# Performance work log

Hardware: AMD Instinct MI355X
Metric: run time of the kernel (lower is better)

## Reference

```python
import jax, jax.numpy as jnp
import numpy as np

HEAD_DIM = 128
N_HEADS = 32
ROPE_DIM = 64
TOPK = 1024
B, S, HID, QLORA = 1, 2048, 4096, 1536
LN_EPS = 1e-5  # torch nn.LayerNorm default


def _hadamard_matrix(n):
    H = np.array([[1.0]], dtype=np.float32)
    while H.shape[0] < n:
        H = np.block([[H, H], [H, -H]])
    return jnp.asarray(H)

_H128 = _hadamard_matrix(HEAD_DIM)
_FWHT_SCALE = HEAD_DIM ** -0.5


def rotate_activation(x):
    # Fast Walsh-Hadamard transform == x @ H_sylvester, scaled by dim**-0.5
    return (x @ _H128) * _FWHT_SCALE


def rope_non_interleaved(x, cos, sin):
    # x: [..., rope_dim]; cos/sin: broadcastable [..., rope_dim/2]
    half = x.shape[-1] // 2
    x1, x2 = x[..., :half], x[..., half:]
    return jnp.concatenate([x1 * cos - x2 * sin, x1 * sin + x2 * cos], axis=-1)


def setup_inputs() -> dict:
    key = jax.random.key(0)
    ks = jax.random.split(key, 8)
    hidden_states = jax.random.normal(ks[0], (B, S, HID), jnp.float32)
    q_compressed = jax.random.normal(ks[1], (B, S, QLORA), jnp.float32)
    # rotary cos/sin for rope_dim=64 (standard concat layout)
    pos = jnp.arange(S, dtype=jnp.float32)
    inv_freq = 1.0 / (10000.0 ** (jnp.arange(0, ROPE_DIM, 2, dtype=jnp.float32) / ROPE_DIM))
    ang = pos[:, None] * inv_freq[None, :]  # [S, 32]
    cos = jnp.tile(jnp.cos(ang), (1, 2))[None]  # [1, S, 64]
    sin = jnp.tile(jnp.sin(ang), (1, 2))[None]
    # additive causal mask [B, S, S]
    causal = jnp.tril(jnp.ones((S, S), jnp.bool_))
    attention_mask = jnp.where(causal, 0.0, -1e9).astype(jnp.float32)[None]
    Wq_b = jax.random.normal(ks[2], (QLORA, N_HEADS * HEAD_DIM), jnp.float32) * (QLORA ** -0.5)
    Wk = jax.random.normal(ks[3], (HID, HEAD_DIM), jnp.float32) * (HID ** -0.5)
    k_gamma = jnp.ones((HEAD_DIM,), jnp.float32)
    k_beta = jnp.zeros((HEAD_DIM,), jnp.float32)
    Ww = jax.random.normal(ks[4], (HID, N_HEADS), jnp.float32) * (HID ** -0.5)
    return {"hidden_states": hidden_states, "q_compressed": q_compressed, "cos": cos,
            "sin": sin, "attention_mask": attention_mask, "Wq_b": Wq_b, "Wk": Wk,
            "k_gamma": k_gamma, "k_beta": k_beta, "Ww": Ww}


def reference(hidden_states, q_compressed, cos, sin, attention_mask, Wq_b, Wk, k_gamma, k_beta, Ww):
    b, s, _ = hidden_states.shape
    softmax_scale = HEAD_DIM ** -0.5
    # queries: [b, s, H, D]
    q = (q_compressed @ Wq_b).reshape(b, s, N_HEADS, HEAD_DIM)
    q_rope, q_nope = q[..., :ROPE_DIM], q[..., ROPE_DIM:]
    # keys: single shared head, LayerNorm(k)
    k = hidden_states @ Wk  # [b, s, D]
    mu = jnp.mean(k, axis=-1, keepdims=True)
    var = jnp.mean(jnp.square(k - mu), axis=-1, keepdims=True)
    k = (k - mu) * jax.lax.rsqrt(var + LN_EPS) * k_gamma + k_beta
    k_rope, k_nope = k[..., :ROPE_DIM], k[..., ROPE_DIM:]
    # non-interleaved RoPE (cos/sin truncated to half_dim=32)
    half = ROPE_DIM // 2
    c, sn = cos[..., :half], sin[..., :half]
    q_rope = rope_non_interleaved(q_rope, c[:, :, None, :], sn[:, :, None, :])
    k_rope = rope_non_interleaved(k_rope, c, sn)
    q = jnp.concatenate([q_rope, q_nope], axis=-1)
    k = jnp.concatenate([k_rope, k_nope], axis=-1)
    # Hadamard activation rotation
    q = rotate_activation(q)
    k = rotate_activation(k)
    # I_{t,s} = sum_h w_{t,h} * ReLU(q_{t,h} . k_s) * scale
    scores = jax.nn.relu(jnp.einsum('bthd,bsd->bths', q, k)) * softmax_scale
    weights = hidden_states @ Ww  # [b, t, H]
    index_scores = jnp.einsum('bths,bth->bts', scores, weights)
    index_scores = index_scores + attention_mask
    topk = min(TOPK, s)
    _, topk_indices = jax.lax.top_k(index_scores, topk)  # [b, s, topk]
    return topk_indices, index_scores
```

## Files before the change

### kernel.cpp

```cpp
#include <hip/hip_runtime.h>
#include <stdint.h>

#define S_LEN 2048
#define HID 4096
#define QLORA 1536
#define NH 32
#define HD 128
#define TOPK_N 1024
#define NEG_INF -1000000000.0f
#define INV_SQRT_HD 0.08838834764831844f

typedef __attribute__((ext_vector_type(8))) short short8;
typedef __attribute__((ext_vector_type(4))) short short4_;
typedef __attribute__((ext_vector_type(4))) float float4_;
typedef __attribute__((ext_vector_type(4))) unsigned uint4_;
typedef __attribute__((ext_vector_type(4))) int int4_;
typedef __attribute__((ext_vector_type(2))) int int2_;

__device__ __forceinline__ short f2bf(float x) {
  union { float f; unsigned u; } v; v.f = x;
  unsigned r = v.u + 0x7FFFu + ((v.u >> 16) & 1u);
  return (short)(r >> 16);
}

__device__ __forceinline__ unsigned f2ord(float x) {
  union { float f; unsigned u; } v; v.f = x;
  return v.u ^ (0x80000000u | (unsigned)((int)v.u >> 31));
}

__device__ __forceinline__ void gload_lds16(const void* g, void* l) {
  __builtin_amdgcn_global_load_lds((const __attribute__((address_space(1))) unsigned int*)g,
                                   (__attribute__((address_space(3))) unsigned int*)l, 16, 0, 0);
}

__global__ __launch_bounds__(256) void prep_kernel(
    const float* __restrict__ hidden, short* __restrict__ hidb,
    const float* __restrict__ qc, char* __restrict__ qc8,
    float* __restrict__ kacc,
    const float* __restrict__ wqb, char* __restrict__ wq8T,
    const float* __restrict__ wk, const float* __restrict__ ww,
    short* __restrict__ kwT) {
  __shared__ __align__(8) char stile[4352];
  int bid = blockIdx.x;
  const int tid = threadIdx.x;
  if (bid < 8192) {
    int i = bid * 256 + tid;
    float4 v = ((const float4*)hidden)[i];
    short4_ o;
    o[0] = f2bf(v.x); o[1] = f2bf(v.y); o[2] = f2bf(v.z); o[3] = f2bf(v.w);
    ((short4_*)hidb)[i] = o;
    return;
  }
  if (bid < 9728) {
    int i = (bid - 8192) * 256 + tid;
    float4 f0 = ((const float4*)qc)[i * 2];
    float4 f1 = ((const float4*)qc)[i * 2 + 1];
    int lo = 0, hi = 0;
    lo = __builtin_amdgcn_cvt_pk_fp8_f32(f0.x, f0.y, lo, 0);
    lo = __builtin_amdgcn_cvt_pk_fp8_f32(f0.z, f0.w, lo, 1);
    hi = __builtin_amdgcn_cvt_pk_fp8_f32(f1.x, f1.y, hi, 0);
    hi = __builtin_amdgcn_cvt_pk_fp8_f32(f1.z, f1.w, hi, 1);
    ((int2_*)qc8)[i] = (int2_){lo, hi};
    return;
  }
  if (bid < 10048) {
    int i = (bid - 9728) * 256 + tid;
    ((float4_*)kacc)[i] = (float4_){0.f, 0.f, 0.f, 0.f};
    return;
  }
  if (bid < 13120) {
    char (*t8)[33] = (char(*)[33])stile;
    int b = bid - 10048;
    int k0 = (b >> 7) * 64, n0 = (b & 127) * 32;
    #pragma unroll
    for (int i = 0; i < 8; i++) {
      int e = tid + i * 256;
      int r = e >> 5, c = e & 31;
      float x = wqb[(size_t)(k0 + r) * HID + n0 + c];
      t8[r][c] = (char)__builtin_amdgcn_cvt_pk_fp8_f32(x, x, 0, 0);
    }
    __syncthreads();
    int nl = tid >> 3, jk = (tid & 7) * 8;
    union { char c[8]; long l; } o;
    #pragma unroll
    for (int j = 0; j < 8; j++) o.c[j] = t8[jk + j][nl];
    *(long*)(wq8T + (size_t)(n0 + nl) * QLORA + k0 + jk) = o.l;
    return;
  }
  short (*tile)[33] = (short(*)[33])stile;
  const float* in; short* out; int R, C, bx, by;
  if (bid < 13632) {
    int b2 = bid - 13120;
    in = wk; out = kwT; R = HID; C = HD; bx = b2 & 3; by = b2 >> 2;
  } else {
    int b3 = bid - 13632;
    in = ww; out = kwT + 128 * HID; R = HID; C = NH; bx = 0; by = b3;
  }
  int c0 = bx * 32, r0 = by * 32;
  int tx = tid & 31, ty = tid >> 5;
  #pragma unroll
  for (int i = 0; i < 32; i += 8)
    tile[ty + i][tx] = f2bf(in[(size_t)(r0 + ty + i) * C + c0 + tx]);
  __syncthreads();
  #pragma unroll
  for (int i = 0; i < 32; i += 8)
    out[(size_t)(c0 + ty + i) * R + r0 + tx] = tile[tx][ty + i];
}

#define QSTAGE8(kt, Ad, Bd) do { \
  _Pragma("unroll") \
  for (int i = 0; i < 4; i++) { \
    int m = w * 32 + i * 8 + lr; \
    int gb = (kt) * 128 + ((lc ^ (m & 7)) << 4); \
    gload_lds16(qc8 + (size_t)(t0 + m) * QLORA + gb, (Ad) + (w * 32 + i * 8) * 128); \
    gload_lds16(wq8T + (size_t)(n0 + m) * QLORA + gb, (Bd) + (w * 32 + i * 8) * 128); \
  } \
} while (0)

#define QCOMPUTE8(Aq, Bq) do { \
  _Pragma("unroll") \
  for (int p = 0; p < 4; p++) { \
    int ch = p * 2 + (quad >> 1); \
    int lo8 = (quad & 1) * 8; \
    long a[2], b[8]; \
    _Pragma("unroll") \
    for (int mt = 0; mt < 2; mt++) { \
      int m = w * 32 + mt * 16 + l15; \
      a[mt] = *(const long*)((Aq) + m * 128 + ((ch ^ (m & 7)) << 4) + lo8); \
    } \
    _Pragma("unroll") \
    for (int nt = 0; nt < 8; nt++) { \
      int n = nt * 16 + l15; \
      b[nt] = *(const long*)((Bq) + n * 128 + ((ch ^ (n & 7)) << 4) + lo8); \
    } \
    _Pragma("unroll") \
    for (int mt = 0; mt < 2; mt++) \
      _Pragma("unroll") \
      for (int nt = 0; nt < 8; nt++) \
        acc[mt][nt] = __builtin_amdgcn_mfma_f32_16x16x32_fp8_fp8(a[mt], b[nt], acc[mt][nt], 0, 0, 0); \
  } \
} while (0)

__global__ __launch_bounds__(256, 2) void gemms_kernel(
    const char* __restrict__ qc8, const char* __restrict__ wq8T,
    const float* __restrict__ cosp, const float* __restrict__ sinp,
    short* __restrict__ qrot,
    const short* __restrict__ hidb, const short* __restrict__ kwT,
    float* __restrict__ kacc) {
  __shared__ __align__(16) char smem[65536];
  const int tid = threadIdx.x;
  const int w = tid >> 6, lane = tid & 63;
  const int l15 = lane & 15, quad = lane >> 4;
  const int lr = lane >> 3, lc = lane & 7;

  if (blockIdx.x < 512) {
    char* A0 = smem;
    char* B0 = smem + 16384;
    char* A1 = smem + 32768;
    char* B1 = smem + 49152;
    const int n0 = (blockIdx.x & 31) * 128;
    const int t0 = (blockIdx.x >> 5) * 128;

    float4_ acc[2][8];
    #pragma unroll
    for (int mt = 0; mt < 2; mt++)
      #pragma unroll
      for (int i = 0; i < 8; i++) acc[mt][i] = (float4_){0.f, 0.f, 0.f, 0.f};

    QSTAGE8(0, A0, B0);
    __syncthreads();
    for (int kt = 0; kt < 12; kt += 2) {
      QSTAGE8(kt + 1, A1, B1);
      QCOMPUTE8(A0, B0);
      __syncthreads();
      if (kt + 2 < 12) QSTAGE8(kt + 2, A0, B0);
      QCOMPUTE8(A1, B1);
      __syncthreads();
    }

    #pragma unroll
    for (int mt = 0; mt < 2; mt++) {
      #pragma unroll
      for (int r = 0; r < 4; r++) {
        const int trow = t0 + w * 32 + mt * 16 + quad * 4 + r;
        float v[8];
        #pragma unroll
        for (int nt = 0; nt < 8; nt++) v[nt] = acc[mt][nt][r];
        float cc0 = cosp[trow * 64 + l15], cc1 = cosp[trow * 64 + 16 + l15];
        float ss0 = sinp[trow * 64 + l15], ss1 = sinp[trow * 64 + 16 + l15];
        float r0 = v[0] * cc0 - v[2] * ss0, r1 = v[1] * cc1 - v[3] * ss1;
        float r2 = v[0] * ss0 + v[2] * cc0, r3 = v[1] * ss1 + v[3] * cc1;
        v[0] = r0; v[1] = r1; v[2] = r2; v[3] = r3;
        short* orow = qrot + (size_t)trow * HID + n0;
        #pragma unroll
        for (int nt = 0; nt < 8; nt++)
          orow[nt * 16 + l15] = f2bf(v[nt]);
      }
    }
  } else {
    short* Al = (short*)smem;
    short* Bl = (short*)(smem + 8192);
    const int b2 = blockIdx.x - 512;
    const int kc0 = (b2 & 7) * 512;
    const int m0g = (b2 >> 3) * 64;

    float4_ acc[10];
    #pragma unroll
    for (int i = 0; i < 10; i++) acc[i] = (float4_){0.f, 0.f, 0.f, 0.f};

    for (int k0 = kc0; k0 < kc0 + 512; k0 += 64) {
      #pragma unroll
      for (int i = 0; i < 2; i++) {
        int m = w * 16 + i * 8 + lr;
        int gk = k0 + ((lc ^ (m & 7)) << 3);
        gload_lds16(hidb + (size_t)(m0g + m) * HID + gk, Al + (w * 16 + i * 8) * 64);
      }
      #pragma unroll
      for (int i = 0; i < 5; i++) {
        int n = w * 40 + i * 8 + lr;
        int gk = k0 + ((lc ^ (n & 7)) << 3);
        gload_lds16(kwT + (size_t)n * HID + gk, Bl + (w * 40 + i * 8) * 64);
      }
      __syncthreads();
      #pragma unroll
      for (int kk = 0; kk < 64; kk += 32) {
        int ca = (kk >> 3) + quad;
        int ma = w * 16 + l15;
        short8 a = *(const short8*)(Al + ma * 64 + ((ca ^ (ma & 7)) << 3));
        #pragma unroll
        for (int nt = 0; nt < 10; nt++) {
          int n = nt * 16 + l15;
          short8 b = *(const short8*)(Bl + n * 64 + ((ca ^ (n & 7)) << 3));
          acc[nt] = __builtin_amdgcn_mfma_f32_16x16x32_bf16(a, b, acc[nt], 0, 0, 0);
        }
      }
      __syncthreads();
    }
    #pragma unroll
    for (int nt = 0; nt < 10; nt++)
      #pragma unroll
      for (int r = 0; r < 4; r++) {
        int row = m0g + w * 16 + quad * 4 + r;
        atomicAdd(&kacc[(size_t)row * 160 + nt * 16 + l15], acc[nt][r]);
      }
  }
}

__global__ __launch_bounds__(256) void ln_rope_kernel(
    const float* __restrict__ kacc, const float* __restrict__ gamma,
    const float* __restrict__ beta, const float* __restrict__ cosp,
    const float* __restrict__ sinp, short* __restrict__ krot) {
  const int tid = threadIdx.x;
  const int row = blockIdx.x * 16 + (tid >> 4);
  const int l16 = tid & 15;
  const int c0 = l16 * 8;
  const float* rp = kacc + (size_t)row * 160 + c0;
  float4 f0 = ((const float4*)rp)[0], f1 = ((const float4*)rp)[1];
  float v[8] = {f0.x, f0.y, f0.z, f0.w, f1.x, f1.y, f1.z, f1.w};
  float s = 0.f, ss = 0.f;
  #pragma unroll
  for (int j = 0; j < 8; j++) { s += v[j]; ss += v[j] * v[j]; }
  #pragma unroll
  for (int d = 1; d <= 8; d <<= 1) {
    s += __shfl_xor(s, d, 64); ss += __shfl_xor(ss, d, 64);
  }
  float mu = s * (1.0f / 128.0f);
  float var = ss * (1.0f / 128.0f) - mu * mu;
  float rs = rsqrtf(var + 1e-5f);
  #pragma unroll
  for (int j = 0; j < 8; j++)
    v[j] = (v[j] - mu) * rs * gamma[c0 + j] + beta[c0 + j];
  #pragma unroll
  for (int j = 0; j < 8; j++) {
    float p = __shfl_xor(v[j], 4, 64);
    if (l16 < 8) {
      int idx = (c0 + j) & 31;
      float c = cosp[row * 64 + idx], sn = sinp[row * 64 + idx];
      v[j] = v[j] * c + p * ((l16 < 4) ? -sn : sn);
    }
  }
  short8 o;
  #pragma unroll
  for (int j = 0; j < 8; j++) o[j] = f2bf(v[j]);
  *(short8*)(krot + (size_t)row * 128 + c0) = o;
}

__global__ __launch_bounds__(256, 2) void scores_kernel(
    const short* __restrict__ qrot, const short* __restrict__ krot,
    const float* __restrict__ kacc, float* __restrict__ isc) {
  __shared__ __align__(16) char smem[65536];
  short* buf0 = (short*)smem;
  short* buf1 = (short*)(smem + 32768);

  const int tid = threadIdx.x;
  const int w = tid >> 6, lane = tid & 63;
  const int l15 = lane & 15, quad = lane >> 4;
  const int wm = w >> 1, wn = w & 1;
  const int lr16 = lane >> 4, lc16 = lane & 15;

  const int bid = blockIdx.x;
  const int strip = (bid & 1) ? (511 - (bid >> 1)) : (bid >> 1);
  const int t0 = strip * 4;
  const int nsb = (t0 + 3) / 128 + 1;

  const short* Abase = qrot + (size_t)t0 * 32 * 128;
  #pragma unroll
  for (int i = 0; i < 8; i++) {
    int m = (w * 8 + i) * 4 + lr16;
    int gofs = m * 128 + ((lc16 ^ (m & 7)) << 3);
    gload_lds16(Abase + gofs, buf0 + (w * 8 + i) * 512);
    gload_lds16(krot + gofs, buf1 + (w * 8 + i) * 512);
  }
  __syncthreads();

  short8 af[4][4];
  #pragma unroll
  for (int k4 = 0; k4 < 4; k4++) {
    int ca = k4 * 4 + quad;
    #pragma unroll
    for (int mt = 0; mt < 4; mt++) {
      int m = wm * 64 + mt * 16 + l15;
      af[k4][mt] = *(const short8*)(buf0 + m * 128 + ((ca ^ (m & 7)) << 3));
    }
  }

  const int t_a = t0 + wm * 2, t_b = t_a + 1;
  float wq[4][4];
  #pragma unroll
  for (int mt = 0; mt < 4; mt++) {
    int tt = (mt < 2) ? t_a : t_b;
    #pragma unroll
    for (int r = 0; r < 4; r++)
      wq[mt][r] = kacc[(size_t)tt * 160 + 128 + (mt & 1) * 16 + quad * 4 + r];
  }
  __syncthreads();

  for (int sb = 0; sb < nsb; sb++) {
    short* cur = (sb & 1) ? buf0 : buf1;
    if (sb + 1 < nsb) {
      short* nxt = (sb & 1) ? buf1 : buf0;
      const short* Bbase = krot + (size_t)(sb + 1) * 128 * 128;
      #pragma unroll
      for (int i = 0; i < 8; i++) {
        int m = (w * 8 + i) * 4 + lr16;
        int gofs = m * 128 + ((lc16 ^ (m & 7)) << 3);
        gload_lds16(Bbase + gofs, nxt + (w * 8 + i) * 512);
      }
    }

    float4_ acc[4][4];
    #pragma unroll
    for (int mt = 0; mt < 4; mt++)
      #pragma unroll
      for (int nt = 0; nt < 4; nt++) acc[mt][nt] = (float4_){0.f, 0.f, 0.f, 0.f};

    #pragma unroll
    for (int k4 = 0; k4 < 4; k4++) {
      int ca = k4 * 4 + quad;
      short8 b[4];
      #pragma unroll
      for (int nt = 0; nt < 4; nt++) {
        int n = wn * 64 + nt * 16 + l15;
        b[nt] = *(const short8*)(cur + n * 128 + ((ca ^ (n & 7)) << 3));
      }
      #pragma unroll
      for (int mt = 0; mt < 4; mt++)
        #pragma unroll
        for (int nt = 0; nt < 4; nt++)
          acc[mt][nt] = __builtin_amdgcn_mfma_f32_16x16x32_bf16(af[k4][mt], b[nt], acc[mt][nt], 0, 0, 0);
    }

    #pragma unroll
    for (int nt = 0; nt < 4; nt++) {
      float pa = 0.f, pb = 0.f;
      #pragma unroll
      for (int r = 0; r < 4; r++) {
        pa += fmaxf(acc[0][nt][r], 0.f) * wq[0][r] + fmaxf(acc[1][nt][r], 0.f) * wq[1][r];
        pb += fmaxf(acc[2][nt][r], 0.f) * wq[2][r] + fmaxf(acc[3][nt][r], 0.f) * wq[3][r];
      }
      pa += __shfl_xor(pa, 16, 64); pa += __shfl_xor(pa, 32, 64);
      pb += __shfl_xor(pb, 16, 64); pb += __shfl_xor(pb, 32, 64);
      int s = sb * 128 + wn * 64 + nt * 16 + l15;
      if (quad == 0)
        isc[(size_t)t_a * S_LEN + s] = (s <= t_a) ? pa * INV_SQRT_HD : NEG_INF;
      else if (quad == 1)
        isc[(size_t)t_b * S_LEN + s] = (s <= t_b) ? pb * INV_SQRT_HD : NEG_INF;
    }

    __syncthreads();
  }

  if (wn == 0) {
    const int myrow = (lane < 32) ? t_a : t_b;
    const int l32 = lane & 31;
    float4_ nf = (float4_){NEG_INF, NEG_INF, NEG_INF, NEG_INF};
    float4_* rowp = (float4_*)(isc + (size_t)myrow * S_LEN);
    for (int i = nsb * 32 + l32; i < 512; i += 32) rowp[i] = nf;
  }
}

#define CEK(x, y, d) { if ((d) ? (v[x] < v[y]) : (v[x] > v[y])) { unsigned _t = v[x]; v[x] = v[y]; v[y] = _t; } }

__device__ __forceinline__ void shfl_phase(unsigned v[8], int j, int base, bool d) {
  const int delta = j >> 3;
  const bool keep_max = (((base & j) == 0) == d);
  #pragma unroll
  for (int r = 0; r < 8; r++) {
    unsigned pv = (unsigned)__shfl_xor((int)v[r], delta, 64);
    unsigned mx = v[r] > pv ? v[r] : pv;
    unsigned mn = v[r] > pv ? pv : v[r];
    v[r] = keep_max ? mx : mn;
  }
}

__device__ __forceinline__ void reg_phase(unsigned v[8], bool d) {
  CEK(0, 4, d); CEK(1, 5, d); CEK(2, 6, d); CEK(3, 7, d);
  CEK(0, 2, d); CEK(1, 3, d); CEK(4, 6, d); CEK(5, 7, d);
  CEK(0, 1, d); CEK(2, 3, d); CEK(4, 5, d); CEK(6, 7, d);
}

__device__ __forceinline__ int chswz(int c) { return c ^ ((c >> 3) & 7); }

__device__ __forceinline__ void lds_phase(unsigned v[8], unsigned* keys, int tid, int base,
                                          int j, bool d) {
  const int c0 = tid * 2, c1 = c0 + 1;
  ((uint4_*)keys)[chswz(c0)] = (uint4_){v[0], v[1], v[2], v[3]};
  ((uint4_*)keys)[chswz(c1)] = (uint4_){v[4], v[5], v[6], v[7]};
  __syncthreads();
  const int ptid = tid ^ (j >> 3);
  uint4_ u0 = ((uint4_*)keys)[chswz(ptid * 2)];
  uint4_ u1 = ((uint4_*)keys)[chswz(ptid * 2 + 1)];
  unsigned p[8] = {u0[0], u0[1], u0[2], u0[3], u1[0], u1[1], u1[2], u1[3]};
  const bool keep_max = (((base & j) == 0) == d);
  #pragma unroll
  for (int r = 0; r < 8; r++) {
    unsigned mx = v[r] > p[r] ? v[r] : p[r];
    unsigned mn = v[r] > p[r] ? p[r] : v[r];
    v[r] = keep_max ? mx : mn;
  }
  __syncthreads();
}

__global__ __launch_bounds__(256) void topk_kernel(const float* __restrict__ isc,
                                                   int* __restrict__ idx_out) {
  __shared__ __align__(16) unsigned keys[2048];
  const int t = blockIdx.x;
  const int tid = threadIdx.x;
  const int base = tid * 8;
  unsigned v[8];
  {
    const float* row = isc + (size_t)t * S_LEN;
    float4 f0 = ((const float4*)row)[tid * 2];
    float4 f1 = ((const float4*)row)[tid * 2 + 1];
    v[0] = (f2ord(f0.x) & 0xFFFFF800u) | (unsigned)(2047 - base - 0);
    v[1] = (f2ord(f0.y) & 0xFFFFF800u) | (unsigned)(2047 - base - 1);
    v[2] = (f2ord(f0.z) & 0xFFFFF800u) | (unsigned)(2047 - base - 2);
    v[3] = (f2ord(f0.w) & 0xFFFFF800u) | (unsigned)(2047 - base - 3);
    v[4] = (f2ord(f1.x) & 0xFFFFF800u) | (unsigned)(2047 - base - 4);
    v[5] = (f2ord(f1.y) & 0xFFFFF800u) | (unsigned)(2047 - base - 5);
    v[6] = (f2ord(f1.z) & 0xFFFFF800u) | (unsigned)(2047 - base - 6);
    v[7] = (f2ord(f1.w) & 0xFFFFF800u) | (unsigned)(2047 - base - 7);
  }
  CEK(0, 1, true); CEK(2, 3, false); CEK(4, 5, true); CEK(6, 7, false);
  CEK(0, 2, true); CEK(1, 3, true); CEK(4, 6, false); CEK(5, 7, false);
  CEK(0, 1, true); CEK(2, 3, true); CEK(4, 5, false); CEK(6, 7, false);
  {
    bool d8 = ((base & 8) == 0);
    CEK(0, 4, d8); CEK(1, 5, d8); CEK(2, 6, d8); CEK(3, 7, d8);
    CEK(0, 2, d8); CEK(1, 3, d8); CEK(4, 6, d8); CEK(5, 7, d8);
    CEK(0, 1, d8); CEK(2, 3, d8); CEK(4, 5, d8); CEK(6, 7, d8);
  }
  #pragma unroll
  for (int kb = 4; kb <= 11; kb++) {
    const int k = 1 << kb;
    const bool d = ((base & k) == 0);
    for (int j = k >> 1; j >= 512; j >>= 1)
      lds_phase(v, keys, tid, base, j, d);
    {
      int jtop = (k >> 1) < 256 ? (k >> 1) : 256;
      for (int j = jtop; j >= 8; j >>= 1)
        shfl_phase(v, j, base, d);
    }
    reg_phase(v, d);
  }
  if (tid < 128) {
    int4_ o0, o1;
    #pragma unroll
    for (int r = 0; r < 4; r++) o0[r] = 2047 - (int)(v[r] & 0x7FFu);
    #pragma unroll
    for (int r = 0; r < 4; r++) o1[r] = 2047 - (int)(v[4 + r] & 0x7FFu);
    ((int4_*)(idx_out + (size_t)t * TOPK_N))[tid * 2] = o0;
    ((int4_*)(idx_out + (size_t)t * TOPK_N))[tid * 2 + 1] = o1;
  }
}

extern "C" void kernel_launch(void* const* d_in, const int* in_sizes, int n_in,
                              void* d_out, int out_size, void* d_ws, size_t ws_size,
                              hipStream_t stream) {
  const float* hidden = (const float*)d_in[0];
  const float* qc     = (const float*)d_in[1];
  const float* cosp   = (const float*)d_in[2];
  const float* sinp   = (const float*)d_in[3];
  const float* wqb    = (const float*)d_in[5];
  const float* wk     = (const float*)d_in[6];
  const float* gamma  = (const float*)d_in[7];
  const float* beta   = (const float*)d_in[8];
  const float* ww     = (const float*)d_in[9];

  char* ws = (char*)d_ws;
  short* hidb = (short*)ws;
  char*  qc8  = (char*)(ws + 16777216);
  char*  wq8T = (char*)(ws + 19922944);
  short* kwT  = (short*)(ws + 26214400);
  short* krot = (short*)(ws + 27525120);
  short* qrot = (short*)(ws + 28049408);
  float* kacc = (float*)(ws + 44826624);

  int*   idx_out = (int*)d_out;
  float* isc     = ((float*)d_out) + (size_t)S_LEN * TOPK_N;

  prep_kernel<<<dim3(13760), dim3(256), 0, stream>>>(hidden, hidb, qc, qc8, kacc,
                                                     wqb, wq8T, wk, ww, kwT);
  gemms_kernel<<<dim3(768), dim3(256), 0, stream>>>(qc8, wq8T, cosp, sinp, qrot,
                                                    hidb, kwT, kacc);
  ln_rope_kernel<<<dim3(128), dim3(256), 0, stream>>>(kacc, gamma, beta, cosp, sinp, krot);
  scores_kernel<<<dim3(512), dim3(256), 0, stream>>>(qrot, krot, kacc, isc);
  topk_kernel<<<dim3(2048), dim3(256), 0, stream>>>(isc, idx_out);
}
```

Before: 244.7 us.

## Store rotated q and k in fp8 and use fp8 MFMA for index scores

The rotated q and k activations are now written as fp8 instead of bf16, and the scores kernel runs fp8 MFMA on byte-sized LDS tiles with a matching swizzle. This halves the q/k traffic and the LDS footprint, which allows three blocks per CU instead of two. The cost is lower precision in the index scores, which could change the top-k selection near ties.

```diff
diff --git a/kernel.cpp b/kernel.cpp
--- a/kernel.cpp
+++ b/kernel.cpp
@@ -26,6 +26,10 @@
 __device__ __forceinline__ unsigned f2ord(float x) {
   union { float f; unsigned u; } v; v.f = x;
   return v.u ^ (0x80000000u | (unsigned)((int)v.u >> 31));
+}
+
+__device__ __forceinline__ char f2fp8(float x) {
+  return (char)__builtin_amdgcn_cvt_pk_fp8_f32(x, x, 0, 0);
 }
 
 __device__ __forceinline__ void gload_lds16(const void* g, void* l) {
@@ -77,7 +81,7 @@
       int e = tid + i * 256;
       int r = e >> 5, c = e & 31;
       float x = wqb[(size_t)(k0 + r) * HID + n0 + c];
-      t8[r][c] = (char)__builtin_amdgcn_cvt_pk_fp8_f32(x, x, 0, 0);
+      t8[r][c] = f2fp8(x);
     }
     __syncthreads();
     int nl = tid >> 3, jk = (tid & 7) * 8;
@@ -144,7 +148,7 @@
 __global__ __launch_bounds__(256, 2) void gemms_kernel(
     const char* __restrict__ qc8, const char* __restrict__ wq8T,
     const float* __restrict__ cosp, const float* __restrict__ sinp,
-    short* __restrict__ qrot,
+    char* __restrict__ qrot8,
     const short* __restrict__ hidb, const short* __restrict__ kwT,
     float* __restrict__ kacc) {
   __shared__ __align__(16) char smem[65536];
@@ -191,10 +195,10 @@
         float r0 = v[0] * cc0 - v[2] * ss0, r1 = v[1] * cc1 - v[3] * ss1;
         float r2 = v[0] * ss0 + v[2] * cc0, r3 = v[1] * ss1 + v[3] * cc1;
         v[0] = r0; v[1] = r1; v[2] = r2; v[3] = r3;
-        short* orow = qrot + (size_t)trow * HID + n0;
+        char* orow = qrot8 + (size_t)trow * HID + n0;
         #pragma unroll
         for (int nt = 0; nt < 8; nt++)
-          orow[nt * 16 + l15] = f2bf(v[nt]);
+          orow[nt * 16 + l15] = f2fp8(v[nt]);
       }
     }
   } else {
@@ -249,7 +253,7 @@
 __global__ __launch_bounds__(256) void ln_rope_kernel(
     const float* __restrict__ kacc, const float* __restrict__ gamma,
     const float* __restrict__ beta, const float* __restrict__ cosp,
-    const float* __restrict__ sinp, short* __restrict__ krot) {
+    const float* __restrict__ sinp, char* __restrict__ krot8) {
   const int tid = threadIdx.x;
   const int row = blockIdx.x * 16 + (tid >> 4);
   const int l16 = tid & 15;
@@ -279,48 +283,51 @@
       v[j] = v[j] * c + p * ((l16 < 4) ? -sn : sn);
     }
   }
-  short8 o;
-  #pragma unroll
-  for (int j = 0; j < 8; j++) o[j] = f2bf(v[j]);
-  *(short8*)(krot + (size_t)row * 128 + c0) = o;
-}
-
-__global__ __launch_bounds__(256, 2) void scores_kernel(
-    const short* __restrict__ qrot, const short* __restrict__ krot,
+  int lo = 0, hi = 0;
+  lo = __builtin_amdgcn_cvt_pk_fp8_f32(v[0], v[1], lo, 0);
+  lo = __builtin_amdgcn_cvt_pk_fp8_f32(v[2], v[3], lo, 1);
+  hi = __builtin_amdgcn_cvt_pk_fp8_f32(v[4], v[5], hi, 0);
+  hi = __builtin_amdgcn_cvt_pk_fp8_f32(v[6], v[7], hi, 1);
+  *(int2_*)(krot8 + (size_t)row * 128 + c0) = (int2_){lo, hi};
+}
+
+__global__ __launch_bounds__(256, 3) void scores_kernel(
+    const char* __restrict__ qrot8, const char* __restrict__ krot8,
     const float* __restrict__ kacc, float* __restrict__ isc) {
-  __shared__ __align__(16) char smem[65536];
-  short* buf0 = (short*)smem;
-  short* buf1 = (short*)(smem + 32768);
+  __shared__ __align__(16) char smem[32768];
+  char* buf0 = smem;
+  char* buf1 = smem + 16384;
 
   const int tid = threadIdx.x;
   const int w = tid >> 6, lane = tid & 63;
   const int l15 = lane & 15, quad = lane >> 4;
   const int wm = w >> 1, wn = w & 1;
-  const int lr16 = lane >> 4, lc16 = lane & 15;
+  const int lr8 = lane >> 3, lc8 = lane & 7;
 
   const int bid = blockIdx.x;
   const int strip = (bid & 1) ? (511 - (bid >> 1)) : (bid >> 1);
   const int t0 = strip * 4;
   const int nsb = (t0 + 3) / 128 + 1;
 
-  const short* Abase = qrot + (size_t)t0 * 32 * 128;
-  #pragma unroll
-  for (int i = 0; i < 8; i++) {
-    int m = (w * 8 + i) * 4 + lr16;
-    int gofs = m * 128 + ((lc16 ^ (m & 7)) << 3);
-    gload_lds16(Abase + gofs, buf0 + (w * 8 + i) * 512);
-    gload_lds16(krot + gofs, buf1 + (w * 8 + i) * 512);
+  const char* Abase = qrot8 + (size_t)t0 * 32 * 128;
+  #pragma unroll
+  for (int i = 0; i < 4; i++) {
+    int m = i * 32 + w * 8 + lr8;
+    int gofs = m * 128 + ((lc8 ^ (m & 7)) << 4);
+    gload_lds16(Abase + gofs, buf0 + (i * 32 + w * 8) * 128);
+    gload_lds16(krot8 + gofs, buf1 + (i * 32 + w * 8) * 128);
   }
   __syncthreads();
 
-  short8 af[4][4];
+  long af[4][4];
   #pragma unroll
   for (int k4 = 0; k4 < 4; k4++) {
-    int ca = k4 * 4 + quad;
+    int ch = k4 * 2 + (quad >> 1);
+    int lo8 = (quad & 1) * 8;
     #pragma unroll
     for (int mt = 0; mt < 4; mt++) {
       int m = wm * 64 + mt * 16 + l15;
-      af[k4][mt] = *(const short8*)(buf0 + m * 128 + ((ca ^ (m & 7)) << 3));
+      af[k4][mt] = *(const long*)(buf0 + m * 128 + ((ch ^ (m & 7)) << 4) + lo8);
     }
   }
 
@@ -336,15 +343,15 @@
   __syncthreads();
 
   for (int sb = 0; sb < nsb; sb++) {
-    short* cur = (sb & 1) ? buf0 : buf1;
+    char* cur = (sb & 1) ? buf0 : buf1;
     if (sb + 1 < nsb) {
-      short* nxt = (sb & 1) ? buf1 : buf0;
-      const short* Bbase = krot + (size_t)(sb + 1) * 128 * 128;
-      #pragma unroll
-      for (int i = 0; i < 8; i++) {
-        int m = (w * 8 + i) * 4 + lr16;
-        int gofs = m * 128 + ((lc16 ^ (m & 7)) << 3);
-        gload_lds16(Bbase + gofs, nxt + (w * 8 + i) * 512);
+      char* nxt = (sb & 1) ? buf1 : buf0;
+      const char* Bbase = krot8 + (size_t)(sb + 1) * 128 * 128;
+      #pragma unroll
+      for (int i = 0; i < 4; i++) {
+        int m = i * 32 + w * 8 + lr8;
+        int gofs = m * 128 + ((lc8 ^ (m & 7)) << 4);
+        gload_lds16(Bbase + gofs, nxt + (i * 32 + w * 8) * 128);
       }
     }
 
@@ -356,18 +363,19 @@
 
     #pragma unroll
     for (int k4 = 0; k4 < 4; k4++) {
-      int ca = k4 * 4 + quad;
-      short8 b[4];
+      int ch = k4 * 2 + (quad >> 1);
+      int lo8 = (quad & 1) * 8;
+      long b[4];
       #pragma unroll
       for (int nt = 0; nt < 4; nt++) {
         int n = wn * 64 + nt * 16 + l15;
-        b[nt] = *(const short8*)(cur + n * 128 + ((ca ^ (n & 7)) << 3));
+        b[nt] = *(const long*)(cur + n * 128 + ((ch ^ (n & 7)) << 4) + lo8);
       }
       #pragma unroll
       for (int mt = 0; mt < 4; mt++)
         #pragma unroll
         for (int nt = 0; nt < 4; nt++)
-          acc[mt][nt] = __builtin_amdgcn_mfma_f32_16x16x32_bf16(af[k4][mt], b[nt], acc[mt][nt], 0, 0, 0);
+          acc[mt][nt] = __builtin_amdgcn_mfma_f32_16x16x32_fp8_fp8(af[k4][mt], b[nt], acc[mt][nt], 0, 0, 0);
     }
 
     #pragma unroll
@@ -508,22 +516,22 @@
   const float* ww     = (const float*)d_in[9];
 
   char* ws = (char*)d_ws;
-  short* hidb = (short*)ws;
-  char*  qc8  = (char*)(ws + 16777216);
-  char*  wq8T = (char*)(ws + 19922944);
-  short* kwT  = (short*)(ws + 26214400);
-  short* krot = (short*)(ws + 27525120);
-  short* qrot = (short*)(ws + 28049408);
-  float* kacc = (float*)(ws + 44826624);
+  short* hidb  = (short*)ws;
+  char*  qc8   = (char*)(ws + 16777216);
+  char*  wq8T  = (char*)(ws + 19922944);
+  short* kwT   = (short*)(ws + 26214400);
+  char*  krot8 = (char*)(ws + 27525120);
+  char*  qrot8 = (char*)(ws + 27787264);
+  float* kacc  = (float*)(ws + 36175872);
 
   int*   idx_out = (int*)d_out;
   float* isc     = ((float*)d_out) + (size_t)S_LEN * TOPK_N;
 
   prep_kernel<<<dim3(13760), dim3(256), 0, stream>>>(hidden, hidb, qc, qc8, kacc,
                                                      wqb, wq8T, wk, ww, kwT);
-  gemms_kernel<<<dim3(768), dim3(256), 0, stream>>>(qc8, wq8T, cosp, sinp, qrot,
+  gemms_kernel<<<dim3(768), dim3(256), 0, stream>>>(qc8, wq8T, cosp, sinp, qrot8,
                                                     hidb, kwT, kacc);
-  ln_rope_kernel<<<dim3(128), dim3(256), 0, stream>>>(kacc, gamma, beta, cosp, sinp, krot);
-  scores_kernel<<<dim3(512), dim3(256), 0, stream>>>(qrot, krot, kacc, isc);
+  ln_rope_kernel<<<dim3(128), dim3(256), 0, stream>>>(kacc, gamma, beta, cosp, sinp, krot8);
+  scores_kernel<<<dim3(512), dim3(256), 0, stream>>>(qrot8, krot8, kacc, isc);
   topk_kernel<<<dim3(2048), dim3(256), 0, stream>>>(isc, idx_out);
 }
```

Result: no change. 248.8 us (+1.6%).
